# Kernel optimization log

Hardware: AMD Instinct MI355X
Metric: run time of the kernel (lower is better)

Reference implementation:

```python
import jax, jax.numpy as jnp
import numpy as np

B, T, V = 4, 2048, 2048
D, H, L = 512, 8, 4
HD = D // H


def setup_inputs() -> dict:
    key = jax.random.key(0)
    ks = jax.random.split(key, 8)
    inp = {
        "x": jax.random.normal(ks[0], (B, T, V), dtype=jnp.float32),
        "token_embedding": jax.random.normal(ks[1], (D, V), dtype=jnp.float32),
        "position_embedding": jax.random.normal(ks[2], (T, D), dtype=jnp.float32),
        "Wk": jax.random.normal(ks[3], (L, D, D), dtype=jnp.float32),
        "Wq": jax.random.normal(ks[4], (L, D, D), dtype=jnp.float32),
        "Wv": jax.random.normal(ks[5], (L, D, D), dtype=jnp.float32),
        "Wp": jax.random.normal(ks[6], (L, D, D), dtype=jnp.float32),
        "readout": jax.random.normal(ks[7], (V, D), dtype=jnp.float32),
    }
    return inp


def _attention_block(h, wk, wq, wv, wp):
    # h: [B, T, D]; weights [D, D] (inner_dim == D since head_dim*num_heads == D)
    b, t, c = h.shape
    s = c ** (-0.5)

    def proj(w):
        # F.linear(h, w) = h @ w.T -> [B,T,D] -> [B,H,T,HD], scaled by C^{-1/2}
        return (jnp.einsum('btc,dc->btd', h, w) * s).reshape(b, t, H, HD).transpose(0, 2, 1, 3)

    q, k, v = proj(wq), proj(wk), proj(wv)
    scores = jnp.einsum('bhqd,bhkd->bhqk', q, k) * (HD ** (-0.5))  # [B,H,T,T]
    attn = jax.nn.softmax(scores, axis=-1)
    out = jnp.einsum('bhqk,bhkd->bhqd', attn, v)  # [B,H,T,HD]
    out = out.transpose(0, 2, 1, 3).reshape(b, t, c)
    # projection.size(-1) == inner_dim == D
    return jnp.einsum('btc,oc->bto', out, wp) * (c ** (-0.5))


def reference(x, token_embedding, position_embedding, Wk, Wq, Wv, Wp, readout):
    b, t, c = x.shape  # c == vocab_size
    tok = jnp.einsum('btv,dv->btd', x, token_embedding) * (c ** (-0.5))
    h = tok + position_embedding[:t]
    for l in range(L):
        h = _attention_block(h, Wk[l], Wq[l], Wv[l], Wp[l])
    # logits on last token; readout.size(-1) == D
    logits = jnp.einsum('bd,vd->bv', h[:, -1, :], readout) * (D ** (-0.5))
    return logits
```

## Files before the change

### kernel.cpp

```cpp
#include <hip/hip_runtime.h>
#include <math.h>

typedef __attribute__((ext_vector_type(4)))  float    f32x4;
typedef __attribute__((ext_vector_type(16))) float    f32x16;
typedef __attribute__((ext_vector_type(2)))  _Float16 f16x2;
typedef __attribute__((ext_vector_type(4)))  _Float16 f16x4;
typedef __attribute__((ext_vector_type(8)))  _Float16 f16x8;
typedef __attribute__((ext_vector_type(4)))  unsigned u32x4;

constexpr int Bc  = 4;
constexpr int Tc  = 2048;
constexpr int Vc  = 2048;
constexpr int Dc  = 512;
constexpr int Hc  = 8;
constexpr int HDc = 64;
constexpr int Lc  = 4;
constexpr size_t SZe = (size_t)Bc * Tc * Dc;

constexpr float SM_C = 12.0f;

__device__ __forceinline__ void gload_lds16(const _Float16* g, _Float16* s) {
    __builtin_amdgcn_global_load_lds(
        (const __attribute__((address_space(1))) void*)g,
        (__attribute__((address_space(3))) void*)s,
        16, 0, 0);
}

__device__ __forceinline__ unsigned cvt_pk_u(float a, float b) {
    return __builtin_bit_cast(unsigned, __builtin_amdgcn_cvt_pkrtz(a, b));
}

__global__ __launch_bounds__(256) void cvt_k(
    const float* __restrict__ in, _Float16* __restrict__ out, int n4)
{
    for (int i = blockIdx.x * 256 + threadIdx.x; i < n4; i += gridDim.x * 256) {
        float4 v = ((const float4*)in)[i];
        f16x4 h = {(_Float16)v.x, (_Float16)v.y, (_Float16)v.z, (_Float16)v.w};
        *(f16x4*)&out[(size_t)i * 4] = h;
    }
}

__global__ __launch_bounds__(256) void cvtW_k(
    const float* __restrict__ a, const float* __restrict__ b,
    const float* __restrict__ c, const float* __restrict__ d,
    _Float16* __restrict__ oa, _Float16* __restrict__ ob,
    _Float16* __restrict__ oc, _Float16* __restrict__ od, int n4)
{
    const float* in; _Float16* out;
    switch (blockIdx.y) {
        case 0:  in = a; out = oa; break;
        case 1:  in = b; out = ob; break;
        case 2:  in = c; out = oc; break;
        default: in = d; out = od; break;
    }
    for (int i = blockIdx.x * 256 + threadIdx.x; i < n4; i += gridDim.x * 256) {
        float4 v = ((const float4*)in)[i];
        f16x4 h = {(_Float16)v.x, (_Float16)v.y, (_Float16)v.z, (_Float16)v.w};
        *(f16x4*)&out[(size_t)i * 4] = h;
    }
}


template<bool QKV>
__global__ __launch_bounds__(256) void gemm_f16(
    const _Float16* __restrict__ A,
    const _Float16* __restrict__ W0, const _Float16* __restrict__ W1,
    const _Float16* __restrict__ W2,
    void* __restrict__ C0, const float* __restrict__ pos,
    int K, float scA, float scB)
{
    __shared__ __align__(16) _Float16 LA[2][128 * 64];
    __shared__ __align__(16) _Float16 LB[2][64 * 64];

    const int tid = threadIdx.x;
    const int w  = tid >> 6, l = tid & 63;
    const int li = l & 15,  lg = l >> 4;
    const int wm = w >> 1,  wn = w & 1;
    const int m0 = blockIdx.x * 128;

    int sec = 0, n0;
    const _Float16* Wb;
    if (QKV) {
        sec = blockIdx.y >> 3; n0 = (blockIdx.y & 7) * 64;
        Wb = (sec == 0) ? W0 : ((sec == 1) ? W1 : W2);
    } else {
        n0 = blockIdx.y * 64; Wb = W0;
    }
    const float scale = (sec == 0) ? scA : scB;

    const _Float16* srcA[4];
    const _Float16* srcB[2];
#pragma unroll
    for (int i = 0; i < 4; ++i) {
        const int d = i * 4096 + tid * 16;
        const int r = d >> 7, cb = (d & 127) ^ ((r & 7) << 4);
        srcA[i] = A + (size_t)(m0 + r) * K + (cb >> 1);
    }
#pragma unroll
    for (int i = 0; i < 2; ++i) {
        const int d = i * 4096 + tid * 16;
        const int r = d >> 7, cb = (d & 127) ^ ((r & 7) << 4);
        srcB[i] = Wb + (size_t)(n0 + r) * K + (cb >> 1);
    }

    auto stage = [&](int b) {
#pragma unroll
        for (int i = 0; i < 4; ++i) { gload_lds16(srcA[i], &LA[b][i * 2048 + tid * 8]); srcA[i] += 64; }
#pragma unroll
        for (int i = 0; i < 2; ++i) { gload_lds16(srcB[i], &LB[b][i * 2048 + tid * 8]); srcB[i] += 64; }
    };

    f32x4 acc[4][2];
#pragma unroll
    for (int i = 0; i < 4; ++i)
#pragma unroll
        for (int j = 0; j < 2; ++j) acc[i][j] = (f32x4){0.f, 0.f, 0.f, 0.f};

    auto compute = [&](int b) {
        const char* Ab = (const char*)&LA[b][0];
        const char* Bb = (const char*)&LB[b][0];
        f16x8 af[4][2], bf[2][2];
#pragma unroll
        for (int mb = 0; mb < 4; ++mb) {
            const int row = wm * 64 + mb * 16 + li, sz = (row & 7) << 4;
#pragma unroll
            for (int fi = 0; fi < 2; ++fi)
                af[mb][fi] = *(const f16x8*)(Ab + row * 128 + ((fi * 64 + lg * 16) ^ sz));
        }
#pragma unroll
        for (int nb = 0; nb < 2; ++nb) {
            const int row = wn * 32 + nb * 16 + li, sz = (row & 7) << 4;
#pragma unroll
            for (int fi = 0; fi < 2; ++fi)
                bf[nb][fi] = *(const f16x8*)(Bb + row * 128 + ((fi * 64 + lg * 16) ^ sz));
        }
#pragma unroll
        for (int mb = 0; mb < 4; ++mb)
#pragma unroll
            for (int nb = 0; nb < 2; ++nb)
#pragma unroll
                for (int fi = 0; fi < 2; ++fi)
                    acc[mb][nb] = __builtin_amdgcn_mfma_f32_16x16x32_f16(
                        af[mb][fi], bf[nb][fi], acc[mb][nb], 0, 0, 0);
    };

    const int NTk = K >> 6;
    stage(0);
    for (int kt = 0; kt < NTk; ++kt) {
        const int cur = kt & 1;
        if (kt + 1 < NTk) {
            stage(cur ^ 1);
            asm volatile("s_waitcnt vmcnt(6)" ::: "memory");
        } else {
            asm volatile("s_waitcnt vmcnt(0)" ::: "memory");
        }
        __builtin_amdgcn_s_barrier();
        __builtin_amdgcn_sched_barrier(0);
        compute(cur);
        __builtin_amdgcn_s_barrier();
        __builtin_amdgcn_sched_barrier(0);
    }

#pragma unroll
    for (int mb = 0; mb < 4; ++mb) {
#pragma unroll
        for (int nb = 0; nb < 2; ++nb) {
            const int mbase = m0 + wm * 64 + mb * 16 + lg * 4;
            const int nc    = n0 + wn * 32 + nb * 16 + li;
            if (QKV && sec == 2) {
                const int t0 = mbase & (Tc - 1);
                const int bh2 = (mbase >> 11) * Hc + (nc >> 6), d = nc & 63;
                f16x4 vv;
#pragma unroll
                for (int r = 0; r < 4; ++r) vv[r] = (_Float16)(acc[mb][nb][r] * scale);
                _Float16* vf = (_Float16*)C0 + 2 * SZe;
                const size_t adr =
                    (((size_t)bh2 * 32 + (t0 >> 6)) * 8 + (d >> 5) * 4 + ((t0 >> 4) & 3)) * 512
                    + ((d & 31) + 32 * ((t0 >> 3) & 1)) * 8 + (t0 & 7);
                *(f16x4*)&vf[adr] = vv;
            } else if (QKV && sec == 1) {
                _Float16* kf = (_Float16*)C0 + SZe;
                const int t0 = mbase & (Tc - 1);
                const int bh2 = (mbase >> 11) * Hc + (nc >> 6), d = nc & 63;
                const size_t adr0 =
                    (((size_t)bh2 * 32 + (t0 >> 6)) * 8 + ((t0 >> 5) & 1) * 4 + (d >> 4)) * 512
                    + ((t0 & 31) + 32 * ((d >> 3) & 1)) * 8 + (d & 7);
#pragma unroll
                for (int r = 0; r < 4; ++r)
                    kf[adr0 + (size_t)r * 8] = (_Float16)(acc[mb][nb][r] * scale);
            } else if (QKV) {
                _Float16* outp = (_Float16*)C0;
#pragma unroll
                for (int r = 0; r < 4; ++r) {
                    const int m = mbase + r, bb2 = m >> 11, t = m & (Tc - 1);
                    outp[(((size_t)bb2 * Hc + (nc >> 6)) * Tc + t) * HDc + (nc & 63)] =
                        (_Float16)(acc[mb][nb][r] * scale);
                }
            } else {
                _Float16* outp = (_Float16*)C0;
#pragma unroll
                for (int r = 0; r < 4; ++r) {
                    const int m = mbase + r;
                    float val = acc[mb][nb][r] * scale;
                    if (pos) val += pos[(size_t)(m & (Tc - 1)) * Dc + nc];
                    outp[(size_t)m * Dc + nc] = (_Float16)val;
                }
            }
        }
    }
}

__global__ __launch_bounds__(256) void attn_mfma(
    const _Float16* __restrict__ Qh, const _Float16* __restrict__ Kf,
    const _Float16* __restrict__ Vf, _Float16* __restrict__ o)
{
    __shared__ float cm[4224];

    const int bid = blockIdx.x;
    const int bh  = bid & 31;
    const int qt  = bid >> 5;
    const int hh  = bh & (Hc - 1);
    const int bb  = bh >> 3;
    const int tid = threadIdx.x;
    const int w   = tid >> 6;
    const int l   = tid & 63;
    const int li  = l & 31, lg2 = l >> 5;
    const int qhalf = w & 1, khalf = w >> 1;
    const int q0  = qt * 64 + qhalf * 32;

    const _Float16* Qb = Qh + (size_t)bh * Tc * HDc;
    f16x8 qf[4];
#pragma unroll
    for (int fi = 0; fi < 4; ++fi)
        qf[fi] = *(const f16x8*)&Qb[(size_t)(q0 + li) * HDc + fi * 16 + lg2 * 8];

    const _Float16* Kb  = Kf + (size_t)bh * Tc * HDc + (khalf * 4) * 512 + l * 8;
    const _Float16* Vb0 = Vf + (size_t)bh * Tc * HDc + (khalf * 2) * 512 + l * 8;
    const _Float16* Vb1 = Vb0 + 4 * 512;

    f32x16 oacc0, oacc1, sinit;
#pragma unroll
    for (int i = 0; i < 16; ++i) { oacc0[i] = 0.f; oacc1[i] = 0.f; sinit[i] = -SM_C; }
    float lrun = 0.f;

    f16x8 kfr[4], vfr[4];
#pragma unroll
    for (int fi = 0; fi < 4; ++fi) kfr[fi] = *(const f16x8*)(Kb + fi * 512);
#pragma unroll
    for (int m = 0; m < 2; ++m) {
        vfr[m]     = *(const f16x8*)(Vb0 + m * 512);
        vfr[2 + m] = *(const f16x8*)(Vb1 + m * 512);
    }
    Kb += 4096; Vb0 += 4096; Vb1 += 4096;

    constexpr int NT = Tc / 64;
    for (int kt = 0; kt < NT; ++kt) {
        __builtin_amdgcn_s_setprio(1);
        f32x16 s = __builtin_amdgcn_mfma_f32_32x32x16_f16(kfr[0], qf[0], sinit, 0, 0, 0);
        s = __builtin_amdgcn_mfma_f32_32x32x16_f16(kfr[1], qf[1], s, 0, 0, 0);
        s = __builtin_amdgcn_mfma_f32_32x32x16_f16(kfr[2], qf[2], s, 0, 0, 0);
        s = __builtin_amdgcn_mfma_f32_32x32x16_f16(kfr[3], qf[3], s, 0, 0, 0);
        __builtin_amdgcn_s_setprio(0);

        if (kt + 1 < NT) {
#pragma unroll
            for (int fi = 0; fi < 4; ++fi) kfr[fi] = *(const f16x8*)(Kb + fi * 512);
            Kb += 4096;
        }
        __builtin_amdgcn_sched_barrier(0);

        unsigned cc[8];
        float ls0 = 0.f, ls1 = 0.f;
#pragma unroll
        for (int g = 0; g < 4; ++g) {
            float p0 = __builtin_amdgcn_exp2f(s[4 * g + 0]);
            float p1 = __builtin_amdgcn_exp2f(s[4 * g + 1]);
            float p2 = __builtin_amdgcn_exp2f(s[4 * g + 2]);
            float p3 = __builtin_amdgcn_exp2f(s[4 * g + 3]);
            ls0 += p0 + p1; ls1 += p2 + p3;
            cc[2 * g]     = cvt_pk_u(p0, p1);
            cc[2 * g + 1] = cvt_pk_u(p2, p3);
        }
        lrun += ls0 + ls1;

        f16x8 Bf[2];
#pragma unroll
        for (int m = 0; m < 2; ++m) {
            auto u = __builtin_amdgcn_permlane32_swap(cc[m * 4 + 0], cc[m * 4 + 2], false, false);
            auto v = __builtin_amdgcn_permlane32_swap(cc[m * 4 + 1], cc[m * 4 + 3], false, false);
            u32x4 b4 = (u32x4){u[0], v[0], u[1], v[1]};
            Bf[m] = __builtin_bit_cast(f16x8, b4);
        }

        __builtin_amdgcn_s_setprio(1);
        oacc0 = __builtin_amdgcn_mfma_f32_32x32x16_f16(vfr[0], Bf[0], oacc0, 0, 0, 0);
        oacc0 = __builtin_amdgcn_mfma_f32_32x32x16_f16(vfr[1], Bf[1], oacc0, 0, 0, 0);
        oacc1 = __builtin_amdgcn_mfma_f32_32x32x16_f16(vfr[2], Bf[0], oacc1, 0, 0, 0);
        oacc1 = __builtin_amdgcn_mfma_f32_32x32x16_f16(vfr[3], Bf[1], oacc1, 0, 0, 0);
        __builtin_amdgcn_s_setprio(0);

        if (kt + 1 < NT) {
#pragma unroll
            for (int m = 0; m < 2; ++m) {
                vfr[m]     = *(const f16x8*)(Vb0 + m * 512);
                vfr[2 + m] = *(const f16x8*)(Vb1 + m * 512);
            }
            Vb0 += 4096; Vb1 += 4096;
        }
        __builtin_amdgcn_sched_barrier(0);
    }

    lrun += __shfl_xor(lrun, 32);
    const int cbase = qhalf * (64 * 33) + l * 33;
    if (khalf == 1) {
#pragma unroll
        for (int i = 0; i < 16; ++i) cm[cbase + i]      = oacc0[i];
#pragma unroll
        for (int i = 0; i < 16; ++i) cm[cbase + 16 + i] = oacc1[i];
        cm[cbase + 32] = lrun;
    }
    __syncthreads();
    if (khalf == 0) {
#pragma unroll
        for (int i = 0; i < 16; ++i) oacc0[i] += cm[cbase + i];
#pragma unroll
        for (int i = 0; i < 16; ++i) oacc1[i] += cm[cbase + 16 + i];
        lrun += cm[cbase + 32];

        const float inv = 1.f / lrun;
        _Float16* op = o + ((size_t)(bb * Tc + q0 + li) * Dc + hh * HDc);
#pragma unroll
        for (int g = 0; g < 4; ++g) {
            const int d0 = 8 * g + 4 * lg2;
            f16x4 r0 = {(_Float16)(oacc0[4 * g + 0] * inv), (_Float16)(oacc0[4 * g + 1] * inv),
                        (_Float16)(oacc0[4 * g + 2] * inv), (_Float16)(oacc0[4 * g + 3] * inv)};
            f16x4 r1 = {(_Float16)(oacc1[4 * g + 0] * inv), (_Float16)(oacc1[4 * g + 1] * inv),
                        (_Float16)(oacc1[4 * g + 2] * inv), (_Float16)(oacc1[4 * g + 3] * inv)};
            *(f16x4*)(op + d0)      = r0;
            *(f16x4*)(op + 32 + d0) = r1;
        }
    }
}

__global__ __launch_bounds__(256) void readout_k(
    const _Float16* __restrict__ h, const float* __restrict__ ro,
    float* __restrict__ out, float scale)
{
    const int idx = blockIdx.x * 256 + threadIdx.x;
    const int vv  = idx & (Vc - 1);
    const int bb  = idx >> 11;
    const _Float16* hp = h + (size_t)(bb * Tc + (Tc - 1)) * Dc;
    const float* rp = ro + (size_t)vv * Dc;
    float ax = 0.f, ay = 0.f, az = 0.f, aw = 0.f;
#pragma unroll 8
    for (int i = 0; i < Dc / 4; ++i) {
        f16x4  hv = *(const f16x4*)(hp + i * 4);
        float4 rv = *(const float4*)(rp + i * 4);
        ax = fmaf((float)hv[0], rv.x, ax);
        ay = fmaf((float)hv[1], rv.y, ay);
        az = fmaf((float)hv[2], rv.z, az);
        aw = fmaf((float)hv[3], rv.w, aw);
    }
    out[idx] = ((ax + ay) + (az + aw)) * scale;
}

extern "C" void kernel_launch(void* const* d_in, const int* in_sizes, int n_in,
                              void* d_out, int out_size, void* d_ws, size_t ws_size,
                              hipStream_t stream)
{
    const float* x    = (const float*)d_in[0];
    const float* temb = (const float*)d_in[1];
    const float* pemb = (const float*)d_in[2];
    const float* Wk   = (const float*)d_in[3];
    const float* Wq   = (const float*)d_in[4];
    const float* Wv   = (const float*)d_in[5];
    const float* Wp   = (const float*)d_in[6];
    const float* ro   = (const float*)d_in[7];
    float* out = (float*)d_out;

    _Float16* h16    = (_Float16*)d_ws;
    _Float16* temb16 = h16 + SZe;
    _Float16* wq16   = temb16 + (size_t)Dc * Vc;
    _Float16* wk16   = wq16 + (size_t)Lc * Dc * Dc;
    _Float16* wv16   = wk16 + (size_t)Lc * Dc * Dc;
    _Float16* wp16   = wv16 + (size_t)Lc * Dc * Dc;
    _Float16* o16    = wp16 + (size_t)Lc * Dc * Dc;
    _Float16* qh     = o16 + SZe;
    _Float16* khF    = qh + SZe;
    _Float16* vhF    = khF + SZe;
    _Float16* x16    = o16;

    const float s_emb  = 1.0f / sqrtf((float)Vc);
    const float s_proj = 1.0f / sqrtf((float)Dc);
    const float s_q    = s_proj * 0.125f * 1.44269504f;

    const int W4 = Lc * Dc * Dc / 4;
    cvt_k<<<2048, 256, 0, stream>>>(x, x16, (int)SZe);
    cvt_k<<<512, 256, 0, stream>>>(temb, temb16, Dc * Vc / 4);
    cvtW_k<<<dim3(512, 4), 256, 0, stream>>>(Wq, Wk, Wv, Wp,
                                             wq16, wk16, wv16, wp16, W4);

    gemm_f16<false><<<dim3(64, 8), 256, 0, stream>>>(
        x16, temb16, nullptr, nullptr, h16, pemb, Vc, s_emb, s_emb);

    const size_t WOFF = (size_t)Dc * Dc;
    for (int lyr = 0; lyr < Lc; ++lyr) {
        gemm_f16<true><<<dim3(64, 24), 256, 0, stream>>>(
            h16, wq16 + lyr * WOFF, wk16 + lyr * WOFF, wv16 + lyr * WOFF,
            qh, nullptr, Dc, s_q, s_proj);

        attn_mfma<<<Bc * Hc * (Tc / 64), 256, 0, stream>>>(qh, khF, vhF, o16);

        gemm_f16<false><<<dim3(64, 8), 256, 0, stream>>>(
            o16, wp16 + lyr * WOFF, nullptr, nullptr, h16, nullptr, Dc, s_proj, s_proj);
    }

    readout_k<<<(Bc * Vc) / 256, 256, 0, stream>>>(h16, ro, out, s_proj);
}
```

Measured before the change: 401.1 us.

## Fuse x fp32-to-fp16 conversion into embedding GEMM and compute softmax sums via MFMA

Adds a dedicated embed_gemm kernel that loads the fp32 input x directly, converts it to fp16 in registers and writes it to LDS, removing the separate conversion kernel and its round trip through memory. The new kernel uses 64x64 tiles, giving twice as many blocks. In attention, the per-lane softmax row-sum additions are replaced by extra MFMAs against a ones vector, and the sched_barriers are dropped. The cost is two extra MFMAs per tile, which competes for matrix throughput, and register-staged A loads in the GEMM.

```diff
diff --git a/kernel.cpp b/kernel.cpp
--- a/kernel.cpp
+++ b/kernel.cpp
@@ -60,6 +60,139 @@
     }
 }
 
+__global__ __launch_bounds__(256) void embed_gemm(
+    const float* __restrict__ A, const _Float16* __restrict__ W,
+    _Float16* __restrict__ C, const float* __restrict__ pos,
+    int K, float scale)
+{
+    __shared__ __align__(16) _Float16 LA[2][64 * 64];
+    __shared__ __align__(16) _Float16 LB[2][64 * 64];
+
+    const int tid = threadIdx.x;
+    const int w  = tid >> 6, l = tid & 63;
+    const int li = l & 15,  lg = l >> 4;
+    const int wm = w >> 1,  wn = w & 1;
+    const int m0 = blockIdx.x * 64;
+    const int n0 = blockIdx.y * 64;
+
+    const float* srcA[2];
+    int wrA[2];
+#pragma unroll
+    for (int c = 0; c < 2; ++c) {
+        const int pb = tid * 32 + c * 16;
+        const int r = pb >> 7, cb = pb & 127;
+        srcA[c] = A + (size_t)(m0 + r) * K + (cb >> 1);
+        wrA[c] = r * 128 + (cb ^ ((r & 7) << 4));
+    }
+    const _Float16* srcB[2];
+#pragma unroll
+    for (int i = 0; i < 2; ++i) {
+        const int d = i * 4096 + tid * 16;
+        const int r = d >> 7, cb = (d & 127) ^ ((r & 7) << 4);
+        srcB[i] = W + (size_t)(n0 + r) * K + (cb >> 1);
+    }
+
+    float4 ra[4];
+    auto issueA = [&]() {
+#pragma unroll
+        for (int c = 0; c < 2; ++c) {
+            ra[2 * c]     = *(const float4*)srcA[c];
+            ra[2 * c + 1] = *(const float4*)(srcA[c] + 4);
+            srcA[c] += 64;
+        }
+    };
+    auto writeA = [&](int b) {
+#pragma unroll
+        for (int c = 0; c < 2; ++c) {
+            f16x8 h = {(_Float16)ra[2*c].x,   (_Float16)ra[2*c].y,
+                       (_Float16)ra[2*c].z,   (_Float16)ra[2*c].w,
+                       (_Float16)ra[2*c+1].x, (_Float16)ra[2*c+1].y,
+                       (_Float16)ra[2*c+1].z, (_Float16)ra[2*c+1].w};
+            *(f16x8*)((char*)&LA[b][0] + wrA[c]) = h;
+        }
+    };
+    auto stageB = [&](int b) {
+#pragma unroll
+        for (int i = 0; i < 2; ++i) { gload_lds16(srcB[i], &LB[b][i * 2048 + tid * 8]); srcB[i] += 64; }
+    };
+
+    f32x4 acc[2][2];
+#pragma unroll
+    for (int i = 0; i < 2; ++i)
+#pragma unroll
+        for (int j = 0; j < 2; ++j) acc[i][j] = (f32x4){0.f, 0.f, 0.f, 0.f};
+
+    auto compute = [&](int b) {
+        const char* Ab = (const char*)&LA[b][0];
+        const char* Bb = (const char*)&LB[b][0];
+        f16x8 af[2][2], bf[2][2];
+#pragma unroll
+        for (int mb = 0; mb < 2; ++mb) {
+            const int row = wm * 32 + mb * 16 + li, sz = (row & 7) << 4;
+#pragma unroll
+            for (int fi = 0; fi < 2; ++fi)
+                af[mb][fi] = *(const f16x8*)(Ab + row * 128 + ((fi * 64 + lg * 16) ^ sz));
+        }
+#pragma unroll
+        for (int nb = 0; nb < 2; ++nb) {
+            const int row = wn * 32 + nb * 16 + li, sz = (row & 7) << 4;
+#pragma unroll
+            for (int fi = 0; fi < 2; ++fi)
+                bf[nb][fi] = *(const f16x8*)(Bb + row * 128 + ((fi * 64 + lg * 16) ^ sz));
+        }
+#pragma unroll
+        for (int mb = 0; mb < 2; ++mb)
+#pragma unroll
+            for (int nb = 0; nb < 2; ++nb)
+#pragma unroll
+                for (int fi = 0; fi < 2; ++fi)
+                    acc[mb][nb] = __builtin_amdgcn_mfma_f32_16x16x32_f16(
+                        af[mb][fi], bf[nb][fi], acc[mb][nb], 0, 0, 0);
+    };
+
+    const int NTk = K >> 6;
+    issueA(); stageB(0);
+    asm volatile("s_waitcnt vmcnt(2)" ::: "memory");
+    writeA(0);
+    asm volatile("s_waitcnt lgkmcnt(0)" ::: "memory");
+
+    for (int kt = 0; kt < NTk; ++kt) {
+        const int cur = kt & 1;
+        const bool more = kt + 1 < NTk;
+        if (more) {
+            issueA();
+            stageB(cur ^ 1);
+            asm volatile("s_waitcnt vmcnt(6)" ::: "memory");
+        } else {
+            asm volatile("s_waitcnt vmcnt(0)" ::: "memory");
+        }
+        __builtin_amdgcn_s_barrier();
+        __builtin_amdgcn_sched_barrier(0);
+        compute(cur);
+        __builtin_amdgcn_s_barrier();
+        __builtin_amdgcn_sched_barrier(0);
+        if (more) {
+            asm volatile("s_waitcnt vmcnt(2)" ::: "memory");
+            writeA(cur ^ 1);
+            asm volatile("s_waitcnt lgkmcnt(0)" ::: "memory");
+        }
+    }
+
+#pragma unroll
+    for (int mb = 0; mb < 2; ++mb) {
+#pragma unroll
+        for (int nb = 0; nb < 2; ++nb) {
+            const int mbase = m0 + wm * 32 + mb * 16 + lg * 4;
+            const int nc    = n0 + wn * 32 + nb * 16 + li;
+#pragma unroll
+            for (int r = 0; r < 4; ++r) {
+                const int m = mbase + r;
+                float val = acc[mb][nb][r] * scale + pos[(size_t)(m & (Tc - 1)) * Dc + nc];
+                C[(size_t)m * Dc + nc] = (_Float16)val;
+            }
+        }
+    }
+}
 
 template<bool QKV>
 __global__ __launch_bounds__(256) void gemm_f16(
@@ -201,9 +334,7 @@
 #pragma unroll
                 for (int r = 0; r < 4; ++r) {
                     const int m = mbase + r;
-                    float val = acc[mb][nb][r] * scale;
-                    if (pos) val += pos[(size_t)(m & (Tc - 1)) * Dc + nc];
-                    outp[(size_t)m * Dc + nc] = (_Float16)val;
+                    outp[(size_t)m * Dc + nc] = (_Float16)(acc[mb][nb][r] * scale);
                 }
             }
         }
@@ -238,10 +369,12 @@
     const _Float16* Vb0 = Vf + (size_t)bh * Tc * HDc + (khalf * 2) * 512 + l * 8;
     const _Float16* Vb1 = Vb0 + 4 * 512;
 
-    f32x16 oacc0, oacc1, sinit;
-#pragma unroll
-    for (int i = 0; i < 16; ++i) { oacc0[i] = 0.f; oacc1[i] = 0.f; sinit[i] = -SM_C; }
-    float lrun = 0.f;
+    f32x16 oacc0, oacc1, lacc, sinit;
+#pragma unroll
+    for (int i = 0; i < 16; ++i) { oacc0[i] = 0.f; oacc1[i] = 0.f; lacc[i] = 0.f; sinit[i] = -SM_C; }
+    f16x8 ones;
+#pragma unroll
+    for (int i = 0; i < 8; ++i) ones[i] = (_Float16)1.f;
 
     f16x8 kfr[4], vfr[4];
 #pragma unroll
@@ -267,21 +400,17 @@
             for (int fi = 0; fi < 4; ++fi) kfr[fi] = *(const f16x8*)(Kb + fi * 512);
             Kb += 4096;
         }
-        __builtin_amdgcn_sched_barrier(0);
 
         unsigned cc[8];
-        float ls0 = 0.f, ls1 = 0.f;
 #pragma unroll
         for (int g = 0; g < 4; ++g) {
             float p0 = __builtin_amdgcn_exp2f(s[4 * g + 0]);
             float p1 = __builtin_amdgcn_exp2f(s[4 * g + 1]);
             float p2 = __builtin_amdgcn_exp2f(s[4 * g + 2]);
             float p3 = __builtin_amdgcn_exp2f(s[4 * g + 3]);
-            ls0 += p0 + p1; ls1 += p2 + p3;
             cc[2 * g]     = cvt_pk_u(p0, p1);
             cc[2 * g + 1] = cvt_pk_u(p2, p3);
         }
-        lrun += ls0 + ls1;
 
         f16x8 Bf[2];
 #pragma unroll
@@ -293,8 +422,10 @@
         }
 
         __builtin_amdgcn_s_setprio(1);
+        lacc  = __builtin_amdgcn_mfma_f32_32x32x16_f16(ones,   Bf[0], lacc,  0, 0, 0);
         oacc0 = __builtin_amdgcn_mfma_f32_32x32x16_f16(vfr[0], Bf[0], oacc0, 0, 0, 0);
         oacc0 = __builtin_amdgcn_mfma_f32_32x32x16_f16(vfr[1], Bf[1], oacc0, 0, 0, 0);
+        lacc  = __builtin_amdgcn_mfma_f32_32x32x16_f16(ones,   Bf[1], lacc,  0, 0, 0);
         oacc1 = __builtin_amdgcn_mfma_f32_32x32x16_f16(vfr[2], Bf[0], oacc1, 0, 0, 0);
         oacc1 = __builtin_amdgcn_mfma_f32_32x32x16_f16(vfr[3], Bf[1], oacc1, 0, 0, 0);
         __builtin_amdgcn_s_setprio(0);
@@ -307,17 +438,16 @@
             }
             Vb0 += 4096; Vb1 += 4096;
         }
-        __builtin_amdgcn_sched_barrier(0);
-    }
-
-    lrun += __shfl_xor(lrun, 32);
+    }
+
+    const float lrun_w = lacc[0];
     const int cbase = qhalf * (64 * 33) + l * 33;
     if (khalf == 1) {
 #pragma unroll
         for (int i = 0; i < 16; ++i) cm[cbase + i]      = oacc0[i];
 #pragma unroll
         for (int i = 0; i < 16; ++i) cm[cbase + 16 + i] = oacc1[i];
-        cm[cbase + 32] = lrun;
+        cm[cbase + 32] = lrun_w;
     }
     __syncthreads();
     if (khalf == 0) {
@@ -325,9 +455,8 @@
         for (int i = 0; i < 16; ++i) oacc0[i] += cm[cbase + i];
 #pragma unroll
         for (int i = 0; i < 16; ++i) oacc1[i] += cm[cbase + 16 + i];
-        lrun += cm[cbase + 32];
-
-        const float inv = 1.f / lrun;
+        const float inv = 1.f / (lrun_w + cm[cbase + 32]);
+
         _Float16* op = o + ((size_t)(bb * Tc + q0 + li) * Dc + hh * HDc);
 #pragma unroll
         for (int g = 0; g < 4; ++g) {
@@ -388,20 +517,17 @@
     _Float16* qh     = o16 + SZe;
     _Float16* khF    = qh + SZe;
     _Float16* vhF    = khF + SZe;
-    _Float16* x16    = o16;
 
     const float s_emb  = 1.0f / sqrtf((float)Vc);
     const float s_proj = 1.0f / sqrtf((float)Dc);
     const float s_q    = s_proj * 0.125f * 1.44269504f;
 
     const int W4 = Lc * Dc * Dc / 4;
-    cvt_k<<<2048, 256, 0, stream>>>(x, x16, (int)SZe);
     cvt_k<<<512, 256, 0, stream>>>(temb, temb16, Dc * Vc / 4);
     cvtW_k<<<dim3(512, 4), 256, 0, stream>>>(Wq, Wk, Wv, Wp,
                                              wq16, wk16, wv16, wp16, W4);
 
-    gemm_f16<false><<<dim3(64, 8), 256, 0, stream>>>(
-        x16, temb16, nullptr, nullptr, h16, pemb, Vc, s_emb, s_emb);
+    embed_gemm<<<dim3(128, 8), 256, 0, stream>>>(x, temb16, h16, pemb, Vc, s_emb);
 
     const size_t WOFF = (size_t)Dc * Dc;
     for (int lyr = 0; lyr < Lc; ++lyr) {
```

Measured after the change: 407.7 us. About the same (+1.6%).

## Compute only last-token queries in final layer; MFMA row-sum for softmax denominator

Applied to the files above, without the earlier changes.

In the last layer only the final token's output feeds the readout, so Q projection, attention and output projection run only for the last 128-row tile of each batch, while K and V are still computed in full. New mstep/moff/ybase and qtoff parameters let the GEMM and attention kernels address those subsets. The attention kernel also computes the softmax denominator with an extra MFMA against a ones vector instead of scalar adds and a shuffle, and drops the sched_barriers. This removes most of the last layer's Q, attention and projection work, at the cost of two extra MFMAs per tile and looser instruction scheduling.

```diff
diff --git a/kernel.cpp b/kernel.cpp
--- a/kernel.cpp
+++ b/kernel.cpp
@@ -67,7 +67,7 @@
     const _Float16* __restrict__ W0, const _Float16* __restrict__ W1,
     const _Float16* __restrict__ W2,
     void* __restrict__ C0, const float* __restrict__ pos,
-    int K, float scA, float scB)
+    int K, float scA, float scB, int mstep, int moff, int ybase)
 {
     __shared__ __align__(16) _Float16 LA[2][128 * 64];
     __shared__ __align__(16) _Float16 LB[2][64 * 64];
@@ -76,15 +76,16 @@
     const int w  = tid >> 6, l = tid & 63;
     const int li = l & 15,  lg = l >> 4;
     const int wm = w >> 1,  wn = w & 1;
-    const int m0 = blockIdx.x * 128;
+    const int m0 = (blockIdx.x * mstep + moff) * 128;
+    const int y  = blockIdx.y + ybase;
 
     int sec = 0, n0;
     const _Float16* Wb;
     if (QKV) {
-        sec = blockIdx.y >> 3; n0 = (blockIdx.y & 7) * 64;
+        sec = y >> 3; n0 = (y & 7) * 64;
         Wb = (sec == 0) ? W0 : ((sec == 1) ? W1 : W2);
     } else {
-        n0 = blockIdx.y * 64; Wb = W0;
+        n0 = y * 64; Wb = W0;
     }
     const float scale = (sec == 0) ? scA : scB;
 
@@ -212,13 +213,13 @@
 
 __global__ __launch_bounds__(256) void attn_mfma(
     const _Float16* __restrict__ Qh, const _Float16* __restrict__ Kf,
-    const _Float16* __restrict__ Vf, _Float16* __restrict__ o)
+    const _Float16* __restrict__ Vf, _Float16* __restrict__ o, int qtoff)
 {
     __shared__ float cm[4224];
 
     const int bid = blockIdx.x;
     const int bh  = bid & 31;
-    const int qt  = bid >> 5;
+    const int qt  = (bid >> 5) + qtoff;
     const int hh  = bh & (Hc - 1);
     const int bb  = bh >> 3;
     const int tid = threadIdx.x;
@@ -238,10 +239,12 @@
     const _Float16* Vb0 = Vf + (size_t)bh * Tc * HDc + (khalf * 2) * 512 + l * 8;
     const _Float16* Vb1 = Vb0 + 4 * 512;
 
-    f32x16 oacc0, oacc1, sinit;
-#pragma unroll
-    for (int i = 0; i < 16; ++i) { oacc0[i] = 0.f; oacc1[i] = 0.f; sinit[i] = -SM_C; }
-    float lrun = 0.f;
+    f32x16 oacc0, oacc1, lacc, sinit;
+#pragma unroll
+    for (int i = 0; i < 16; ++i) { oacc0[i] = 0.f; oacc1[i] = 0.f; lacc[i] = 0.f; sinit[i] = -SM_C; }
+    f16x8 ones;
+#pragma unroll
+    for (int i = 0; i < 8; ++i) ones[i] = (_Float16)1.f;
 
     f16x8 kfr[4], vfr[4];
 #pragma unroll
@@ -267,21 +270,17 @@
             for (int fi = 0; fi < 4; ++fi) kfr[fi] = *(const f16x8*)(Kb + fi * 512);
             Kb += 4096;
         }
-        __builtin_amdgcn_sched_barrier(0);
 
         unsigned cc[8];
-        float ls0 = 0.f, ls1 = 0.f;
 #pragma unroll
         for (int g = 0; g < 4; ++g) {
             float p0 = __builtin_amdgcn_exp2f(s[4 * g + 0]);
             float p1 = __builtin_amdgcn_exp2f(s[4 * g + 1]);
             float p2 = __builtin_amdgcn_exp2f(s[4 * g + 2]);
             float p3 = __builtin_amdgcn_exp2f(s[4 * g + 3]);
-            ls0 += p0 + p1; ls1 += p2 + p3;
             cc[2 * g]     = cvt_pk_u(p0, p1);
             cc[2 * g + 1] = cvt_pk_u(p2, p3);
         }
-        lrun += ls0 + ls1;
 
         f16x8 Bf[2];
 #pragma unroll
@@ -293,8 +292,10 @@
         }
 
         __builtin_amdgcn_s_setprio(1);
+        lacc  = __builtin_amdgcn_mfma_f32_32x32x16_f16(ones,   Bf[0], lacc,  0, 0, 0);
         oacc0 = __builtin_amdgcn_mfma_f32_32x32x16_f16(vfr[0], Bf[0], oacc0, 0, 0, 0);
         oacc0 = __builtin_amdgcn_mfma_f32_32x32x16_f16(vfr[1], Bf[1], oacc0, 0, 0, 0);
+        lacc  = __builtin_amdgcn_mfma_f32_32x32x16_f16(ones,   Bf[1], lacc,  0, 0, 0);
         oacc1 = __builtin_amdgcn_mfma_f32_32x32x16_f16(vfr[2], Bf[0], oacc1, 0, 0, 0);
         oacc1 = __builtin_amdgcn_mfma_f32_32x32x16_f16(vfr[3], Bf[1], oacc1, 0, 0, 0);
         __builtin_amdgcn_s_setprio(0);
@@ -307,17 +308,16 @@
             }
             Vb0 += 4096; Vb1 += 4096;
         }
-        __builtin_amdgcn_sched_barrier(0);
-    }
-
-    lrun += __shfl_xor(lrun, 32);
+    }
+
+    const float lrun_w = lacc[0];
     const int cbase = qhalf * (64 * 33) + l * 33;
     if (khalf == 1) {
 #pragma unroll
         for (int i = 0; i < 16; ++i) cm[cbase + i]      = oacc0[i];
 #pragma unroll
         for (int i = 0; i < 16; ++i) cm[cbase + 16 + i] = oacc1[i];
-        cm[cbase + 32] = lrun;
+        cm[cbase + 32] = lrun_w;
     }
     __syncthreads();
     if (khalf == 0) {
@@ -325,9 +325,8 @@
         for (int i = 0; i < 16; ++i) oacc0[i] += cm[cbase + i];
 #pragma unroll
         for (int i = 0; i < 16; ++i) oacc1[i] += cm[cbase + 16 + i];
-        lrun += cm[cbase + 32];
-
-        const float inv = 1.f / lrun;
+        const float inv = 1.f / (lrun_w + cm[cbase + 32]);
+
         _Float16* op = o + ((size_t)(bb * Tc + q0 + li) * Dc + hh * HDc);
 #pragma unroll
         for (int g = 0; g < 4; ++g) {
@@ -401,18 +400,35 @@
                                              wq16, wk16, wv16, wp16, W4);
 
     gemm_f16<false><<<dim3(64, 8), 256, 0, stream>>>(
-        x16, temb16, nullptr, nullptr, h16, pemb, Vc, s_emb, s_emb);
+        x16, temb16, nullptr, nullptr, h16, pemb, Vc, s_emb, s_emb, 1, 0, 0);
 
     const size_t WOFF = (size_t)Dc * Dc;
     for (int lyr = 0; lyr < Lc; ++lyr) {
-        gemm_f16<true><<<dim3(64, 24), 256, 0, stream>>>(
-            h16, wq16 + lyr * WOFF, wk16 + lyr * WOFF, wv16 + lyr * WOFF,
-            qh, nullptr, Dc, s_q, s_proj);
-
-        attn_mfma<<<Bc * Hc * (Tc / 64), 256, 0, stream>>>(qh, khF, vhF, o16);
-
-        gemm_f16<false><<<dim3(64, 8), 256, 0, stream>>>(
-            o16, wp16 + lyr * WOFF, nullptr, nullptr, h16, nullptr, Dc, s_proj, s_proj);
+        const bool last = (lyr == Lc - 1);
+        if (!last) {
+            gemm_f16<true><<<dim3(64, 24), 256, 0, stream>>>(
+                h16, wq16 + lyr * WOFF, wk16 + lyr * WOFF, wv16 + lyr * WOFF,
+                qh, nullptr, Dc, s_q, s_proj, 1, 0, 0);
+
+            attn_mfma<<<Bc * Hc * (Tc / 64), 256, 0, stream>>>(qh, khF, vhF, o16, 0);
+
+            gemm_f16<false><<<dim3(64, 8), 256, 0, stream>>>(
+                o16, wp16 + lyr * WOFF, nullptr, nullptr, h16, nullptr,
+                Dc, s_proj, s_proj, 1, 0, 0);
+        } else {
+            gemm_f16<true><<<dim3(64, 16), 256, 0, stream>>>(
+                h16, wq16 + lyr * WOFF, wk16 + lyr * WOFF, wv16 + lyr * WOFF,
+                qh, nullptr, Dc, s_q, s_proj, 1, 0, 8);
+            gemm_f16<true><<<dim3(4, 8), 256, 0, stream>>>(
+                h16, wq16 + lyr * WOFF, wk16 + lyr * WOFF, wv16 + lyr * WOFF,
+                qh, nullptr, Dc, s_q, s_proj, 16, 15, 0);
+
+            attn_mfma<<<Bc * Hc, 256, 0, stream>>>(qh, khF, vhF, o16, 31);
+
+            gemm_f16<false><<<dim3(4, 8), 256, 0, stream>>>(
+                o16, wp16 + lyr * WOFF, nullptr, nullptr, h16, nullptr,
+                Dc, s_proj, s_proj, 16, 15, 0);
+        }
     }
 
     readout_k<<<(Bc * Vc) / 256, 256, 0, stream>>>(h16, ro, out, s_proj);
```

Result: faster. 383.0 us (-4.5%).
